# Kernel optimization log

Measured on AMD Instinct MI355X. Metric: run time of the kernel, lower is better.

## Reference

```python
import jax, jax.numpy as jnp
import numpy as np
import math

D_MODEL = 1024
N_HEADS = 16
HEAD_DIM = D_MODEL // N_HEADS  # 64
SEQ_LEN = 4096
LINFORMER_K = 128
BATCH = 4


def setup_inputs() -> dict:
    key = jax.random.key(0)
    ks = jax.random.split(key, 8)
    s = 0.02  # small init so softmax is not saturated
    return {
        "x": jax.random.normal(ks[0], (BATCH, SEQ_LEN, D_MODEL), dtype=jnp.float32),
        "Wq": jax.random.normal(ks[1], (D_MODEL, D_MODEL), dtype=jnp.float32) * s,
        "bq": jnp.zeros((D_MODEL,), dtype=jnp.float32),
        "Wk": jax.random.normal(ks[2], (D_MODEL, D_MODEL), dtype=jnp.float32) * s,
        "bk": jnp.zeros((D_MODEL,), dtype=jnp.float32),
        "Wv": jax.random.normal(ks[3], (D_MODEL, D_MODEL), dtype=jnp.float32) * s,
        "bv": jnp.zeros((D_MODEL,), dtype=jnp.float32),
        "E": jax.random.normal(ks[4], (N_HEADS, LINFORMER_K, SEQ_LEN), dtype=jnp.float32) * s,
    }


def _split_heads(X):
    # [b, l, d_model] -> [b, h, l, head_dim]
    b, l, _ = X.shape
    return X.reshape(b, l, N_HEADS, HEAD_DIM).transpose(0, 2, 1, 3)


def reference(x, Wq, bq, Wk, bk, Wv, bv, E):
    # Projections (nn.Linear: x @ W.T + b)
    Q = _split_heads(x @ Wq.T + bq)  # [b, h, l, hd]
    K = _split_heads(x @ Wk.T + bk)
    V = _split_heads(x @ Wv.T + bv)
    b, h, l, d = Q.shape
    # l == SEQ_LEN so no padding needed (pad branch is a no-op here)
    # Low-rank projection of K/V along sequence: E [h, k, l]
    Kp = jnp.einsum('hkl,bhld->bhkd', E, K)  # [b, h, k, hd]
    Vp = jnp.einsum('hkl,bhld->bhkd', E, V)
    # Small-context attention
    dot = jnp.einsum('bhld,bhkd->bhlk', Q, Kp) / math.sqrt(HEAD_DIM)
    attn = jax.nn.softmax(dot, axis=-1)  # [b, h, l, k]
    Xo = jnp.einsum('bhlk,bhkd->bhld', attn, Vp)
    # combine heads: [b, h, l, hd] -> [b, l, d_model]
    out = Xo.transpose(0, 2, 1, 3).reshape(b, l, h * d)
    return out
```

## Files before the change

kernel.cpp:

```cpp
#include <hip/hip_runtime.h>

typedef __bf16 bf16x8 __attribute__((ext_vector_type(8)));
typedef float f32x4 __attribute__((ext_vector_type(4)));

#define AS1 __attribute__((address_space(1)))
#define AS3 __attribute__((address_space(3)))

__device__ __forceinline__ void gload_lds16(const void* g, void* l) {
    __builtin_amdgcn_global_load_lds((const AS1 void*)g, (AS3 void*)l, 16, 0, 0);
}

__device__ __forceinline__ unsigned short f2bf(float f) {
    unsigned u = __builtin_bit_cast(unsigned, f);
    u += 0x7fffu + ((u >> 16) & 1u);
    return (unsigned short)(u >> 16);
}

__device__ __forceinline__ float bf2f(unsigned short u) {
    return __builtin_bit_cast(float, (unsigned)u << 16);
}

__global__ __launch_bounds__(256) void fused_cvt(
        const float* __restrict__ x, const float* __restrict__ Wq,
        const float* __restrict__ Wk, const float* __restrict__ Wv,
        const float* __restrict__ E,
        unsigned short* __restrict__ xb, unsigned short* __restrict__ xT,
        unsigned short* __restrict__ Wb, unsigned short* __restrict__ Eb) {
    __shared__ unsigned short tile[64][68];
    const int id = blockIdx.x, t = threadIdx.x;
    if (id < 4096) {
        const int cx = id & 15, ly = (id >> 4) & 63, b = id >> 10;
        const int l0 = ly * 64, c0 = cx * 64;
        const int r = t >> 4, c4 = t & 15;
#pragma unroll
        for (int p = 0; p < 4; p++) {
            int row = p * 16 + r;
            const float4 v = *(const float4*)&x[(size_t)(b * 4096 + l0 + row) * 1024 + c0 + c4 * 4];
            ushort4 o;
            o.x = f2bf(v.x); o.y = f2bf(v.y); o.z = f2bf(v.z); o.w = f2bf(v.w);
            *(ushort4*)&xb[(size_t)(b * 4096 + l0 + row) * 1024 + c0 + c4 * 4] = o;
            tile[c4 * 4 + 0][row] = o.x;
            tile[c4 * 4 + 1][row] = o.y;
            tile[c4 * 4 + 2][row] = o.z;
            tile[c4 * 4 + 3][row] = o.w;
        }
        __syncthreads();
#pragma unroll
        for (int p = 0; p < 4; p++) {
            int c = p * 16 + r;
            ushort4 o = *(const ushort4*)&tile[c][c4 * 4];
            *(ushort4*)&xT[(size_t)(b * 1024 + c0 + c) * 4096 + l0 + c4 * 4] = o;
        }
    } else if (id < 7168) {
        const int wi = id - 4096, which = wi >> 10;
        const int i = (wi & 1023) * 256 + t;
        const float* src = (which == 0) ? Wq : (which == 1 ? Wk : Wv);
        float4 v = reinterpret_cast<const float4*>(src)[i];
        ushort4 o;
        o.x = f2bf(v.x); o.y = f2bf(v.y); o.z = f2bf(v.z); o.w = f2bf(v.w);
        reinterpret_cast<ushort4*>(Wb + (size_t)which * 1048576)[i] = o;
    } else {
        const int i = (id - 7168) * 256 + t;
        float4 v = reinterpret_cast<const float4*>(E)[i];
        ushort4 o;
        o.x = f2bf(v.x); o.y = f2bf(v.y); o.z = f2bf(v.z); o.w = f2bf(v.w);
        reinterpret_cast<ushort4*>(Eb)[i] = o;
    }
}

__global__ __launch_bounds__(256) void gemm_ex(
        const unsigned short* __restrict__ Eb, const unsigned short* __restrict__ xTb,
        unsigned short* __restrict__ Exb) {
    __shared__ unsigned short lA[2 * 128 * 32];
    __shared__ unsigned short lB[2 * 128 * 32];
    const int tid = threadIdx.x, w = tid >> 6, lane = tid & 63;
    const int m0 = blockIdx.y * 128, n0 = blockIdx.x * 128;
    const unsigned short* xT = xTb + (size_t)blockIdx.z * 1024 * 4096;
    unsigned short* Ex = Exb + (size_t)blockIdx.z * 2048 * 1024;
    const int srow = lane >> 2, scol = (lane & 3) * 8;
    const int l15 = lane & 15, quad = lane >> 4;
    const int wm = w >> 1, wn = w & 1;
    f32x4 acc[4][4] = {};
    for (int k0 = 0; k0 < 4096; k0 += 64) {
        __syncthreads();
#pragma unroll
        for (int s = 0; s < 2; s++) {
#pragma unroll
            for (int i = 0; i < 2; i++) {
                int t = w * 2 + i;
                gload_lds16(Eb + (size_t)(m0 + t * 16 + srow) * 4096 + k0 + s * 32 + scol,
                            (char*)lA + (s * 8192 + t * 1024));
                gload_lds16(xT + (size_t)(n0 + t * 16 + srow) * 4096 + k0 + s * 32 + scol,
                            (char*)lB + (s * 8192 + t * 1024));
            }
        }
        __syncthreads();
#pragma unroll
        for (int s = 0; s < 2; s++) {
            bf16x8 af[4], bfr[4];
#pragma unroll
            for (int mi = 0; mi < 4; mi++)
                af[mi] = *(const bf16x8*)&lA[(s * 128 + wm * 64 + mi * 16 + l15) * 32 + quad * 8];
#pragma unroll
            for (int ni = 0; ni < 4; ni++)
                bfr[ni] = *(const bf16x8*)&lB[(s * 128 + wn * 64 + ni * 16 + l15) * 32 + quad * 8];
#pragma unroll
            for (int mi = 0; mi < 4; mi++)
#pragma unroll
                for (int ni = 0; ni < 4; ni++)
                    acc[mi][ni] = __builtin_amdgcn_mfma_f32_16x16x32_bf16(af[mi], bfr[ni],
                                                                          acc[mi][ni], 0, 0, 0);
        }
    }
#pragma unroll
    for (int ni = 0; ni < 4; ni++) {
        int col = n0 + wn * 64 + ni * 16 + l15;
#pragma unroll
        for (int mi = 0; mi < 4; mi++) {
            int row = m0 + wm * 64 + mi * 16 + quad * 4;
#pragma unroll
            for (int r = 0; r < 4; r++)
                Ex[(size_t)(row + r) * 1024 + col] = f2bf(acc[mi][ni][r]);
        }
    }
}

__global__ __launch_bounds__(256) void gemm_q(
        const unsigned short* __restrict__ xb, const unsigned short* __restrict__ Wb,
        const float* __restrict__ bq, unsigned short* __restrict__ Qb) {
    __shared__ unsigned short lA[2 * 128 * 32];
    __shared__ unsigned short lB[2 * 128 * 32];
    const int tid = threadIdx.x, w = tid >> 6, lane = tid & 63;
    const int m0 = blockIdx.y * 128, n0 = blockIdx.x * 128;
    const int srow = lane >> 2, scol = (lane & 3) * 8;
    const int l15 = lane & 15, quad = lane >> 4;
    const int wm = w >> 1, wn = w & 1;
    f32x4 acc[4][4] = {};
    for (int k0 = 0; k0 < 1024; k0 += 64) {
        __syncthreads();
#pragma unroll
        for (int s = 0; s < 2; s++) {
#pragma unroll
            for (int i = 0; i < 2; i++) {
                int t = w * 2 + i;
                gload_lds16(xb + (size_t)(m0 + t * 16 + srow) * 1024 + k0 + s * 32 + scol,
                            (char*)lA + (s * 8192 + t * 1024));
                gload_lds16(Wb + (size_t)(n0 + t * 16 + srow) * 1024 + k0 + s * 32 + scol,
                            (char*)lB + (s * 8192 + t * 1024));
            }
        }
        __syncthreads();
#pragma unroll
        for (int s = 0; s < 2; s++) {
            bf16x8 af[4], bfr[4];
#pragma unroll
            for (int mi = 0; mi < 4; mi++)
                af[mi] = *(const bf16x8*)&lA[(s * 128 + wm * 64 + mi * 16 + l15) * 32 + quad * 8];
#pragma unroll
            for (int ni = 0; ni < 4; ni++)
                bfr[ni] = *(const bf16x8*)&lB[(s * 128 + wn * 64 + ni * 16 + l15) * 32 + quad * 8];
#pragma unroll
            for (int mi = 0; mi < 4; mi++)
#pragma unroll
                for (int ni = 0; ni < 4; ni++)
                    acc[mi][ni] = __builtin_amdgcn_mfma_f32_16x16x32_bf16(af[mi], bfr[ni],
                                                                          acc[mi][ni], 0, 0, 0);
        }
    }
#pragma unroll
    for (int ni = 0; ni < 4; ni++) {
        int col = n0 + wn * 64 + ni * 16 + l15;
        float bias_v = bq[col];
#pragma unroll
        for (int mi = 0; mi < 4; mi++) {
            int row = m0 + wm * 64 + mi * 16 + quad * 4;
#pragma unroll
            for (int r = 0; r < 4; r++)
                Qb[(size_t)(row + r) * 1024 + col] = f2bf(acc[mi][ni][r] + bias_v);
        }
    }
}

__global__ __launch_bounds__(256) void kpvp4(
        const unsigned short* __restrict__ Exb, const unsigned short* __restrict__ Wb,
        const unsigned short* __restrict__ Eb, const float* __restrict__ bk,
        const float* __restrict__ bv,
        unsigned short* __restrict__ Kpb, unsigned short* __restrict__ VpTb) {
    __shared__ unsigned short Exsh[2 * 32 * 32];
    __shared__ unsigned short Wksh[2 * 64 * 32];
    __shared__ unsigned short Wvsh[2 * 64 * 32];
    __shared__ float EsumSh[32];
    const int tid = threadIdx.x, w = tid >> 6, lane = tid & 63;
    const int l15 = lane & 15, quad = lane >> 4;
    const int srow = lane >> 2, scol = (lane & 3) * 8;
    const int bh = blockIdx.x & 63, q = blockIdx.x >> 6;
    const int b = bh >> 4, h = bh & 15;
    const unsigned short* Ex = Exb + ((size_t)b * 2048 + h * 128 + q * 32) * 1024;
    const unsigned short* Wk = Wb + 1048576 + (size_t)h * 64 * 1024;
    const unsigned short* Wv = Wb + 2097152 + (size_t)h * 64 * 1024;
    for (int r = w; r < 32; r += 4) {
        const unsigned short* er = Eb + ((size_t)(h * 128 + q * 32 + r)) * 4096;
        float s = 0.f;
#pragma unroll
        for (int i = 0; i < 8; i++) {
            ushort4 a = *(const ushort4*)&er[i * 512 + lane * 8];
            ushort4 b2 = *(const ushort4*)&er[i * 512 + lane * 8 + 4];
            s += bf2f(a.x) + bf2f(a.y) + bf2f(a.z) + bf2f(a.w);
            s += bf2f(b2.x) + bf2f(b2.y) + bf2f(b2.z) + bf2f(b2.w);
        }
#pragma unroll
        for (int off = 32; off >= 1; off >>= 1) s += __shfl_xor(s, off, 64);
        if (lane == 0) EsumSh[r] = s;
    }
    f32x4 accK[4] = {};
    f32x4 accV[2][2] = {};
    auto STAGE = [&](int t, int s) {
        const int c0 = t * 32;
        if (w < 2)
            gload_lds16(Ex + (size_t)(w * 16 + srow) * 1024 + c0 + scol,
                        (char*)Exsh + s * 2048 + w * 1024);
        gload_lds16(Wk + (size_t)(w * 16 + srow) * 1024 + c0 + scol,
                    (char*)Wksh + s * 4096 + w * 1024);
        gload_lds16(Wv + (size_t)(w * 16 + srow) * 1024 + c0 + scol,
                    (char*)Wvsh + s * 4096 + w * 1024);
    };
    auto COMPUTE = [&](int s) {
        if (w < 2) {
            bf16x8 af = *(const bf16x8*)&Exsh[s * 1024 + (w * 16 + l15) * 32 + quad * 8];
#pragma unroll
            for (int nt = 0; nt < 4; nt++) {
                bf16x8 bb = *(const bf16x8*)&Wksh[s * 2048 + (nt * 16 + l15) * 32 + quad * 8];
                accK[nt] = __builtin_amdgcn_mfma_f32_16x16x32_bf16(af, bb, accK[nt], 0, 0, 0);
            }
        } else {
            bf16x8 av[2], be[2];
#pragma unroll
            for (int mi = 0; mi < 2; mi++)
                av[mi] = *(const bf16x8*)&Wvsh[s * 2048 + (((w - 2) * 2 + mi) * 16 + l15) * 32 + quad * 8];
#pragma unroll
            for (int n = 0; n < 2; n++)
                be[n] = *(const bf16x8*)&Exsh[s * 1024 + (n * 16 + l15) * 32 + quad * 8];
#pragma unroll
            for (int mi = 0; mi < 2; mi++)
#pragma unroll
                for (int n = 0; n < 2; n++)
                    accV[mi][n] = __builtin_amdgcn_mfma_f32_16x16x32_bf16(av[mi], be[n],
                                                                          accV[mi][n], 0, 0, 0);
        }
    };
    STAGE(0, 0);
    __syncthreads();
    for (int t = 0; t < 31; ++t) {
        STAGE(t + 1, (t + 1) & 1);
        COMPUTE(t & 1);
        __syncthreads();
    }
    COMPUTE(1);
    unsigned short* Kp = Kpb + (size_t)bh * 128 * 64;
    unsigned short* VpT = VpTb + (size_t)bh * 64 * 128;
    if (w < 2) {
#pragma unroll
        for (int nt = 0; nt < 4; nt++) {
            int col = nt * 16 + l15;
            float bkv = bk[h * 64 + col];
#pragma unroll
            for (int r = 0; r < 4; r++) {
                int krow = w * 16 + quad * 4 + r;
                Kp[(q * 32 + krow) * 64 + col] = f2bf(accK[nt][r] + EsumSh[krow] * bkv);
            }
        }
    } else {
#pragma unroll
        for (int mi = 0; mi < 2; mi++)
#pragma unroll
            for (int n = 0; n < 2; n++) {
                int kcol = n * 16 + l15;
                float es = EsumSh[kcol];
#pragma unroll
                for (int r = 0; r < 4; r++) {
                    int d = ((w - 2) * 2 + mi) * 16 + quad * 4 + r;
                    VpT[d * 128 + q * 32 + kcol] = f2bf(accV[mi][n][r] + es * bv[h * 64 + d]);
                }
            }
    }
}

__global__ __launch_bounds__(256) void attn_kernel(
        const unsigned short* __restrict__ Qb, const unsigned short* __restrict__ Kpb,
        const unsigned short* __restrict__ VpTb, float* __restrict__ out) {
    __shared__ unsigned short P[4 * 16 * 136];
    const int tid = threadIdx.x, w = tid >> 6, lane = tid & 63;
    const int l15 = lane & 15, quad = lane >> 4;
    const int bh = blockIdx.y, b = bh >> 4, h = bh & 15;
    const int l0 = blockIdx.x * 64 + w * 16;
    const unsigned short* Qrow = Qb + (size_t)(b * 4096 + l0 + l15) * 1024 + h * 64;
    bf16x8 aq0 = *(const bf16x8*)&Qrow[quad * 8];
    bf16x8 aq1 = *(const bf16x8*)&Qrow[32 + quad * 8];
    const unsigned short* Kp = Kpb + (size_t)bh * 128 * 64;
    f32x4 acc[8];
#pragma unroll
    for (int kt = 0; kt < 8; kt++) {
        const unsigned short* kr = Kp + (size_t)(kt * 16 + l15) * 64;
        bf16x8 b0 = *(const bf16x8*)&kr[quad * 8];
        bf16x8 b1 = *(const bf16x8*)&kr[32 + quad * 8];
        f32x4 a = {};
        a = __builtin_amdgcn_mfma_f32_16x16x32_bf16(aq0, b0, a, 0, 0, 0);
        a = __builtin_amdgcn_mfma_f32_16x16x32_bf16(aq1, b1, a, 0, 0, 0);
        acc[kt] = a;
    }
    const float scale = 0.125f;
    float pr[8][4];
#pragma unroll
    for (int r = 0; r < 4; r++) {
        float m = -1e30f;
#pragma unroll
        for (int kt = 0; kt < 8; kt++) m = fmaxf(m, acc[kt][r]);
#pragma unroll
        for (int off = 8; off >= 1; off >>= 1) m = fmaxf(m, __shfl_xor(m, off, 64));
        float s = 0.f;
#pragma unroll
        for (int kt = 0; kt < 8; kt++) {
            float e = __expf(scale * (acc[kt][r] - m));
            pr[kt][r] = e;
            s += e;
        }
#pragma unroll
        for (int off = 8; off >= 1; off >>= 1) s += __shfl_xor(s, off, 64);
        float rinv = 1.0f / s;
#pragma unroll
        for (int kt = 0; kt < 8; kt++) pr[kt][r] *= rinv;
    }
    unsigned short* Pw = &P[w * 16 * 136];
#pragma unroll
    for (int kt = 0; kt < 8; kt++)
#pragma unroll
        for (int r = 0; r < 4; r++)
            Pw[(quad * 4 + r) * 136 + kt * 16 + l15] = f2bf(pr[kt][r]);
    __syncthreads();
    bf16x8 ap[4];
#pragma unroll
    for (int t = 0; t < 4; t++)
        ap[t] = *(const bf16x8*)&Pw[l15 * 136 + t * 32 + quad * 8];
    const unsigned short* Vp = VpTb + (size_t)bh * 64 * 128;
    f32x4 acco[4] = {};
#pragma unroll
    for (int nt = 0; nt < 4; nt++) {
        const unsigned short* vr = Vp + (size_t)(nt * 16 + l15) * 128;
#pragma unroll
        for (int t = 0; t < 4; t++) {
            bf16x8 bv = *(const bf16x8*)&vr[t * 32 + quad * 8];
            acco[nt] = __builtin_amdgcn_mfma_f32_16x16x32_bf16(ap[t], bv, acco[nt], 0, 0, 0);
        }
    }
#pragma unroll
    for (int nt = 0; nt < 4; nt++) {
        int col = h * 64 + nt * 16 + l15;
#pragma unroll
        for (int r = 0; r < 4; r++)
            out[(size_t)(b * 4096 + l0 + quad * 4 + r) * 1024 + col] = acco[nt][r];
    }
}

extern "C" void kernel_launch(void* const* d_in, const int* in_sizes, int n_in,
                              void* d_out, int out_size, void* d_ws, size_t ws_size,
                              hipStream_t stream) {
    const float* x  = (const float*)d_in[0];
    const float* Wq = (const float*)d_in[1];
    const float* bq = (const float*)d_in[2];
    const float* Wk = (const float*)d_in[3];
    const float* bk = (const float*)d_in[4];
    const float* Wv = (const float*)d_in[5];
    const float* bv = (const float*)d_in[6];
    const float* E  = (const float*)d_in[7];
    float* out = (float*)d_out;
    char* ws = (char*)d_ws;

    unsigned short* xb   = (unsigned short*)(ws);
    unsigned short* xTb  = (unsigned short*)(ws + 33554432);
    unsigned short* Wb   = (unsigned short*)(ws + 67108864);
    unsigned short* Qb   = (unsigned short*)(ws + 73400320);
    unsigned short* Eb   = (unsigned short*)(ws + 106954752);
    unsigned short* Exb  = (unsigned short*)(ws + 123731968);
    unsigned short* Kpb  = (unsigned short*)(ws + 140509184);
    unsigned short* VpTb = (unsigned short*)(ws + 141557760);
    if (ws_size < 142606336) return;

    fused_cvt<<<15360, 256, 0, stream>>>(x, Wq, Wk, Wv, E, xb, xTb, Wb, Eb);
    gemm_ex<<<dim3(8, 16, 4), 256, 0, stream>>>(Eb, xTb, Exb);
    gemm_q<<<dim3(8, 128), 256, 0, stream>>>(xb, Wb, bq, Qb);
    kpvp4<<<256, 256, 0, stream>>>(Exb, Wb, Eb, bk, bv, Kpb, VpTb);
    attn_kernel<<<dim3(64, 64), 256, 0, stream>>>(Qb, Kpb, VpTb, out);
}
```

Baseline: 380.7 us.

## Fuse Q projection GEMM with low-rank attention in one kernel

Merges the Q projection GEMM and the attention kernel so each 128x128 Q tile is written into LDS with its bias and consumed there, with no round trip through global memory. Each wave handles 64 rows of one head, running QKp^T, softmax and PVp for four 16-row slabs, reusing LDS for the P staging. This drops a 32 MB bf16 write and read of Q plus one launch. In exchange it uses more registers (16 output accumulators plus the GEMM accumulators), which may lower occupancy, and it re-reads Kp/Vp from global per wave.

```diff
diff --git a/kernel.cpp b/kernel.cpp
--- a/kernel.cpp
+++ b/kernel.cpp
@@ -121,62 +121,6 @@
 #pragma unroll
             for (int r = 0; r < 4; r++)
                 Ex[(size_t)(row + r) * 1024 + col] = f2bf(acc[mi][ni][r]);
-        }
-    }
-}
-
-__global__ __launch_bounds__(256) void gemm_q(
-        const unsigned short* __restrict__ xb, const unsigned short* __restrict__ Wb,
-        const float* __restrict__ bq, unsigned short* __restrict__ Qb) {
-    __shared__ unsigned short lA[2 * 128 * 32];
-    __shared__ unsigned short lB[2 * 128 * 32];
-    const int tid = threadIdx.x, w = tid >> 6, lane = tid & 63;
-    const int m0 = blockIdx.y * 128, n0 = blockIdx.x * 128;
-    const int srow = lane >> 2, scol = (lane & 3) * 8;
-    const int l15 = lane & 15, quad = lane >> 4;
-    const int wm = w >> 1, wn = w & 1;
-    f32x4 acc[4][4] = {};
-    for (int k0 = 0; k0 < 1024; k0 += 64) {
-        __syncthreads();
-#pragma unroll
-        for (int s = 0; s < 2; s++) {
-#pragma unroll
-            for (int i = 0; i < 2; i++) {
-                int t = w * 2 + i;
-                gload_lds16(xb + (size_t)(m0 + t * 16 + srow) * 1024 + k0 + s * 32 + scol,
-                            (char*)lA + (s * 8192 + t * 1024));
-                gload_lds16(Wb + (size_t)(n0 + t * 16 + srow) * 1024 + k0 + s * 32 + scol,
-                            (char*)lB + (s * 8192 + t * 1024));
-            }
-        }
-        __syncthreads();
-#pragma unroll
-        for (int s = 0; s < 2; s++) {
-            bf16x8 af[4], bfr[4];
-#pragma unroll
-            for (int mi = 0; mi < 4; mi++)
-                af[mi] = *(const bf16x8*)&lA[(s * 128 + wm * 64 + mi * 16 + l15) * 32 + quad * 8];
-#pragma unroll
-            for (int ni = 0; ni < 4; ni++)
-                bfr[ni] = *(const bf16x8*)&lB[(s * 128 + wn * 64 + ni * 16 + l15) * 32 + quad * 8];
-#pragma unroll
-            for (int mi = 0; mi < 4; mi++)
-#pragma unroll
-                for (int ni = 0; ni < 4; ni++)
-                    acc[mi][ni] = __builtin_amdgcn_mfma_f32_16x16x32_bf16(af[mi], bfr[ni],
-                                                                          acc[mi][ni], 0, 0, 0);
-        }
-    }
-#pragma unroll
-    for (int ni = 0; ni < 4; ni++) {
-        int col = n0 + wn * 64 + ni * 16 + l15;
-        float bias_v = bq[col];
-#pragma unroll
-        for (int mi = 0; mi < 4; mi++) {
-            int row = m0 + wm * 64 + mi * 16 + quad * 4;
-#pragma unroll
-            for (int r = 0; r < 4; r++)
-                Qb[(size_t)(row + r) * 1024 + col] = f2bf(acc[mi][ni][r] + bias_v);
         }
     }
 }
@@ -285,80 +229,144 @@
     }
 }
 
-__global__ __launch_bounds__(256) void attn_kernel(
-        const unsigned short* __restrict__ Qb, const unsigned short* __restrict__ Kpb,
-        const unsigned short* __restrict__ VpTb, float* __restrict__ out) {
-    __shared__ unsigned short P[4 * 16 * 136];
+__global__ __launch_bounds__(256) void gemm_qattn(
+        const unsigned short* __restrict__ xb, const unsigned short* __restrict__ Wb,
+        const float* __restrict__ bq,
+        const unsigned short* __restrict__ Kpb, const unsigned short* __restrict__ VpTb,
+        float* __restrict__ out) {
+    __shared__ __align__(16) unsigned short smem[17408];
+    unsigned short* lA = smem;
+    unsigned short* lB = smem + 8192;
     const int tid = threadIdx.x, w = tid >> 6, lane = tid & 63;
+    const int m0 = blockIdx.y * 128, n0 = blockIdx.x * 128;
+    const int srow = lane >> 2, scol = (lane & 3) * 8;
     const int l15 = lane & 15, quad = lane >> 4;
-    const int bh = blockIdx.y, b = bh >> 4, h = bh & 15;
-    const int l0 = blockIdx.x * 64 + w * 16;
-    const unsigned short* Qrow = Qb + (size_t)(b * 4096 + l0 + l15) * 1024 + h * 64;
-    bf16x8 aq0 = *(const bf16x8*)&Qrow[quad * 8];
-    bf16x8 aq1 = *(const bf16x8*)&Qrow[32 + quad * 8];
-    const unsigned short* Kp = Kpb + (size_t)bh * 128 * 64;
-    f32x4 acc[8];
-#pragma unroll
-    for (int kt = 0; kt < 8; kt++) {
-        const unsigned short* kr = Kp + (size_t)(kt * 16 + l15) * 64;
-        bf16x8 b0 = *(const bf16x8*)&kr[quad * 8];
-        bf16x8 b1 = *(const bf16x8*)&kr[32 + quad * 8];
-        f32x4 a = {};
-        a = __builtin_amdgcn_mfma_f32_16x16x32_bf16(aq0, b0, a, 0, 0, 0);
-        a = __builtin_amdgcn_mfma_f32_16x16x32_bf16(aq1, b1, a, 0, 0, 0);
-        acc[kt] = a;
-    }
+    const int wm = w >> 1, wn = w & 1;
+    f32x4 acc[4][4] = {};
+    for (int k0 = 0; k0 < 1024; k0 += 64) {
+        __syncthreads();
+#pragma unroll
+        for (int s = 0; s < 2; s++) {
+#pragma unroll
+            for (int i = 0; i < 2; i++) {
+                int t = w * 2 + i;
+                gload_lds16(xb + (size_t)(m0 + t * 16 + srow) * 1024 + k0 + s * 32 + scol,
+                            (char*)lA + (s * 8192 + t * 1024));
+                gload_lds16(Wb + (size_t)(n0 + t * 16 + srow) * 1024 + k0 + s * 32 + scol,
+                            (char*)lB + (s * 8192 + t * 1024));
+            }
+        }
+        __syncthreads();
+#pragma unroll
+        for (int s = 0; s < 2; s++) {
+            bf16x8 af[4], bfr[4];
+#pragma unroll
+            for (int mi = 0; mi < 4; mi++)
+                af[mi] = *(const bf16x8*)&lA[(s * 128 + wm * 64 + mi * 16 + l15) * 32 + quad * 8];
+#pragma unroll
+            for (int ni = 0; ni < 4; ni++)
+                bfr[ni] = *(const bf16x8*)&lB[(s * 128 + wn * 64 + ni * 16 + l15) * 32 + quad * 8];
+#pragma unroll
+            for (int mi = 0; mi < 4; mi++)
+#pragma unroll
+                for (int ni = 0; ni < 4; ni++)
+                    acc[mi][ni] = __builtin_amdgcn_mfma_f32_16x16x32_bf16(af[mi], bfr[ni],
+                                                                          acc[mi][ni], 0, 0, 0);
+        }
+    }
+    __syncthreads();
+#pragma unroll
+    for (int ni = 0; ni < 4; ni++) {
+        int lc = wn * 64 + ni * 16 + l15;
+        float bias_v = bq[n0 + lc];
+#pragma unroll
+        for (int mi = 0; mi < 4; mi++) {
+            int lr = wm * 64 + mi * 16 + quad * 4;
+#pragma unroll
+            for (int r = 0; r < 4; r++)
+                smem[(lr + r) * 136 + lc] = f2bf(acc[mi][ni][r] + bias_v);
+        }
+    }
+    __syncthreads();
+    bf16x8 aq[4][2];
+#pragma unroll
+    for (int rt = 0; rt < 4; rt++)
+#pragma unroll
+        for (int ds = 0; ds < 2; ds++)
+            aq[rt][ds] = *(const bf16x8*)&smem[(wm * 64 + rt * 16 + l15) * 136 +
+                                               wn * 64 + ds * 32 + quad * 8];
+    __syncthreads();
+    const int b = m0 >> 12;
+    const int h = blockIdx.x * 2 + wn;
+    const int lbase = (m0 & 4095) + wm * 64;
+    const unsigned short* Kp = Kpb + (size_t)(b * 16 + h) * 128 * 64;
+    const unsigned short* Vp = VpTb + (size_t)(b * 16 + h) * 64 * 128;
     const float scale = 0.125f;
-    float pr[8][4];
-#pragma unroll
-    for (int r = 0; r < 4; r++) {
-        float m = -1e30f;
-#pragma unroll
-        for (int kt = 0; kt < 8; kt++) m = fmaxf(m, acc[kt][r]);
-#pragma unroll
-        for (int off = 8; off >= 1; off >>= 1) m = fmaxf(m, __shfl_xor(m, off, 64));
-        float s = 0.f;
+    f32x4 acco[4][4] = {};
+#pragma unroll
+    for (int rt = 0; rt < 4; rt++) {
+        f32x4 sc[8];
 #pragma unroll
         for (int kt = 0; kt < 8; kt++) {
-            float e = __expf(scale * (acc[kt][r] - m));
-            pr[kt][r] = e;
-            s += e;
-        }
-#pragma unroll
-        for (int off = 8; off >= 1; off >>= 1) s += __shfl_xor(s, off, 64);
-        float rinv = 1.0f / s;
-#pragma unroll
-        for (int kt = 0; kt < 8; kt++) pr[kt][r] *= rinv;
-    }
-    unsigned short* Pw = &P[w * 16 * 136];
-#pragma unroll
-    for (int kt = 0; kt < 8; kt++)
-#pragma unroll
-        for (int r = 0; r < 4; r++)
-            Pw[(quad * 4 + r) * 136 + kt * 16 + l15] = f2bf(pr[kt][r]);
-    __syncthreads();
-    bf16x8 ap[4];
-#pragma unroll
-    for (int t = 0; t < 4; t++)
-        ap[t] = *(const bf16x8*)&Pw[l15 * 136 + t * 32 + quad * 8];
-    const unsigned short* Vp = VpTb + (size_t)bh * 64 * 128;
-    f32x4 acco[4] = {};
-#pragma unroll
-    for (int nt = 0; nt < 4; nt++) {
-        const unsigned short* vr = Vp + (size_t)(nt * 16 + l15) * 128;
-#pragma unroll
-        for (int t = 0; t < 4; t++) {
-            bf16x8 bv = *(const bf16x8*)&vr[t * 32 + quad * 8];
-            acco[nt] = __builtin_amdgcn_mfma_f32_16x16x32_bf16(ap[t], bv, acco[nt], 0, 0, 0);
-        }
-    }
-#pragma unroll
-    for (int nt = 0; nt < 4; nt++) {
-        int col = h * 64 + nt * 16 + l15;
-#pragma unroll
-        for (int r = 0; r < 4; r++)
-            out[(size_t)(b * 4096 + l0 + quad * 4 + r) * 1024 + col] = acco[nt][r];
-    }
+            const unsigned short* kr = Kp + (size_t)(kt * 16 + l15) * 64;
+            bf16x8 b0 = *(const bf16x8*)&kr[quad * 8];
+            bf16x8 b1 = *(const bf16x8*)&kr[32 + quad * 8];
+            f32x4 a = {};
+            a = __builtin_amdgcn_mfma_f32_16x16x32_bf16(aq[rt][0], b0, a, 0, 0, 0);
+            a = __builtin_amdgcn_mfma_f32_16x16x32_bf16(aq[rt][1], b1, a, 0, 0, 0);
+            sc[kt] = a;
+        }
+#pragma unroll
+        for (int r = 0; r < 4; r++) {
+            float m = -1e30f;
+#pragma unroll
+            for (int kt = 0; kt < 8; kt++) m = fmaxf(m, sc[kt][r]);
+#pragma unroll
+            for (int off = 8; off >= 1; off >>= 1) m = fmaxf(m, __shfl_xor(m, off, 64));
+            float s = 0.f;
+#pragma unroll
+            for (int kt = 0; kt < 8; kt++) {
+                float e = __expf(scale * (sc[kt][r] - m));
+                sc[kt][r] = e;
+                s += e;
+            }
+#pragma unroll
+            for (int off = 8; off >= 1; off >>= 1) s += __shfl_xor(s, off, 64);
+            float rinv = 1.0f / s;
+#pragma unroll
+            for (int kt = 0; kt < 8; kt++) sc[kt][r] *= rinv;
+        }
+        unsigned short* slab = smem + (w * 2 + (rt & 1)) * 2176;
+#pragma unroll
+        for (int kt = 0; kt < 8; kt++)
+#pragma unroll
+            for (int r = 0; r < 4; r++)
+                slab[(quad * 4 + r) * 136 + kt * 16 + l15] = f2bf(sc[kt][r]);
+        bf16x8 ap[4];
+#pragma unroll
+        for (int t = 0; t < 4; t++)
+            ap[t] = *(const bf16x8*)&slab[l15 * 136 + t * 32 + quad * 8];
+#pragma unroll
+        for (int nt = 0; nt < 4; nt++) {
+            const unsigned short* vr = Vp + (size_t)(nt * 16 + l15) * 128;
+#pragma unroll
+            for (int t = 0; t < 4; t++) {
+                bf16x8 bv = *(const bf16x8*)&vr[t * 32 + quad * 8];
+                acco[rt][nt] = __builtin_amdgcn_mfma_f32_16x16x32_bf16(ap[t], bv,
+                                                                       acco[rt][nt], 0, 0, 0);
+            }
+        }
+    }
+#pragma unroll
+    for (int rt = 0; rt < 4; rt++)
+#pragma unroll
+        for (int nt = 0; nt < 4; nt++) {
+            int col = h * 64 + nt * 16 + l15;
+#pragma unroll
+            for (int r = 0; r < 4; r++)
+                out[(size_t)(b * 4096 + lbase + rt * 16 + quad * 4 + r) * 1024 + col] =
+                    acco[rt][nt][r];
+        }
 }
 
 extern "C" void kernel_launch(void* const* d_in, const int* in_sizes, int n_in,
@@ -378,7 +386,6 @@
     unsigned short* xb   = (unsigned short*)(ws);
     unsigned short* xTb  = (unsigned short*)(ws + 33554432);
     unsigned short* Wb   = (unsigned short*)(ws + 67108864);
-    unsigned short* Qb   = (unsigned short*)(ws + 73400320);
     unsigned short* Eb   = (unsigned short*)(ws + 106954752);
     unsigned short* Exb  = (unsigned short*)(ws + 123731968);
     unsigned short* Kpb  = (unsigned short*)(ws + 140509184);
@@ -387,7 +394,6 @@
 
     fused_cvt<<<15360, 256, 0, stream>>>(x, Wq, Wk, Wv, E, xb, xTb, Wb, Eb);
     gemm_ex<<<dim3(8, 16, 4), 256, 0, stream>>>(Eb, xTb, Exb);
-    gemm_q<<<dim3(8, 128), 256, 0, stream>>>(xb, Wb, bq, Qb);
     kpvp4<<<256, 256, 0, stream>>>(Exb, Wb, Eb, bk, bv, Kpb, VpTb);
-    attn_kernel<<<dim3(64, 64), 256, 0, stream>>>(Qb, Kpb, VpTb, out);
-}
+    gemm_qattn<<<dim3(8, 128), 256, 0, stream>>>(xb, Wb, bq, Kpb, VpTb, out);
+}
```

Measured after the change: 376.5 us. About the same (-1.1%).
